# Kernel optimization log

Measured on AMD Instinct MI355X. Metric: run time of the kernel, lower is better.

Reference implementation:

```python
import jax, jax.numpy as jnp
import numpy as np
from jax import lax

# Module config (matches init_kwargs)
KH, KW = 2, 3          # kernel_size
C_IN = 64              # in_channels
C_HID = 256            # hidden_channels (4 * in_channels since in_channels <= 96)
C_OUT = 2 * C_IN       # affine transform -> (mu, log_scale)
DN = ('NCHW', 'OIHW', 'NCHW')


def setup_inputs() -> dict:
    key = jax.random.key(0)
    k0, k1, k2 = jax.random.split(key, 3)
    B, H, W = 32, 64, 64
    x = jax.random.normal(k0, (B, C_IN, H, W), dtype=jnp.float32)
    # masked (shifted) conv weights, order 'A' (height-causal)
    Wm = jax.random.normal(k1, (C_HID, C_IN, KH, KW), dtype=jnp.float32) * 0.05
    bm = jnp.zeros((C_HID,), dtype=jnp.float32)
    # 1x1 projection to transform params
    W1 = jax.random.normal(k2, (C_OUT, C_HID, 1, 1), dtype=jnp.float32) * 0.05
    b1 = jnp.zeros((C_OUT,), dtype=jnp.float32)
    return {"x": x, "Wm": Wm, "bm": bm, "W1": W1, "b1": b1}


def _mcf_block(x, Wm, bm, W1, b1):
    """MCFBlock: shifted masked conv (order 'A') -> ReLU -> 1x1 conv.

    Order 'A' causality: output at (h, w) depends only on input rows
    h-KH .. h-1 (strictly above) and columns w-(KW//2) .. w+(KW//2).
    Implemented by padding KH rows on top, (KW-1)//2 cols on each side,
    dropping the last row, then a VALID conv.
    """
    H = x.shape[2]
    cW = (KW - 1) // 2
    xp = jnp.pad(x, ((0, 0), (0, 0), (KH, 0), (cW, cW)))[:, :, :H + KH - 1]
    c = lax.conv_general_dilated(xp, Wm, (1, 1), 'VALID', dimension_numbers=DN)
    c = jax.nn.relu(c + bm[None, :, None, None])
    p = lax.conv_general_dilated(c, W1, (1, 1), 'VALID', dimension_numbers=DN)
    return p + b1[None, :, None, None]


def reference(x, Wm, bm, W1, b1):
    # params -> (mu, scale) for the affine flow (alpha = 1.0)
    params = _mcf_block(x, Wm, bm, W1, b1)      # [B, 2*C_IN, H, W]
    mu, log_scale = jnp.split(params, 2, axis=1)
    scale = jax.nn.sigmoid(log_scale + 2.0)     # macow affine parameterization
    out = scale * x + mu                        # [B, C_IN, H, W]
    logdet = jnp.sum(jnp.log(scale), axis=(1, 2, 3))  # [B]
    return out, logdet
```

## Files before the change

kernel.cpp:

```cpp
#include <hip/hip_runtime.h>
#include <math.h>


#define BATCH 32
#define HDIM 64
#define WDIM 64
#define ROWS 4
#define STRIPS 16
#define NBLK (BATCH * STRIPS)
#define CT_LD 264

typedef __attribute__((ext_vector_type(8))) short short8;
typedef __attribute__((ext_vector_type(4))) float f32x4;

__device__ inline unsigned short f2bf(float f) {
    union { float f; unsigned int u; } v; v.f = f;
    unsigned int u = v.u;
    unsigned int r = u + 0x7FFFu + ((u >> 16) & 1u);
    return (unsigned short)(r >> 16);
}

__device__ inline int xt_off(int slot, int wp, int ci) {
    return ((slot * 66 + wp) << 6) + ((((ci >> 3) ^ (wp & 7)) << 3) | (ci & 7));
}

__global__ __launch_bounds__(256) void mcf_prep(
    const float* __restrict__ Wm, const float* __restrict__ W1,
    unsigned short* __restrict__ WmR, unsigned short* __restrict__ W1b)
{
    int idx = blockIdx.x * 256 + threadIdx.x;
    if (idx < 6 * 256 * 64) {
        int khkw = idx >> 14;
        int rem = idx & 16383;
        int co = rem >> 6;
        int ci = rem & 63;
        int kh = khkw / 3, kw = khkw % 3;
        WmR[idx] = f2bf(Wm[((co * 64 + ci) * 2 + kh) * 3 + kw]);
    } else {
        int i = idx - 6 * 256 * 64;
        W1b[i] = f2bf(W1[i]);
    }
}

__global__ __launch_bounds__(512, 2) void mcf_mfma(
    const float* __restrict__ x,
    const unsigned short* __restrict__ WmR,
    const float* __restrict__ bm,
    const unsigned short* __restrict__ W1b,
    const float* __restrict__ b1,
    float* __restrict__ out, float* __restrict__ row_ld)
{
    __shared__ __align__(16) unsigned short Xt[5 * 66 * 64];
    __shared__ __align__(16) unsigned short Ct[64 * CT_LD];
    __shared__ float red[8];

    const int blk = blockIdx.x;
    const int b = blk >> 4;
    const int h0 = (blk & 15) * ROWS;
    const int tid = threadIdx.x;
    const int lane = tid & 63;
    const int wv = tid >> 6;
    const int col = lane & 15;
    const int g = lane >> 4;

    for (int l = tid; l < 640; l += 512) {
        int s = l >> 7, rr = l & 127;
        int wp = (rr >= 64) ? 65 : 0, ci = rr & 63;
        Xt[xt_off(s, wp, ci)] = 0;
    }
    #pragma unroll
    for (int it = 0; it < 40; ++it) {
        int idx = it * 512 + tid;
        int w = idx & 63;
        int ci = (idx >> 6) & 63;
        int slot = idx >> 12;
        int row = h0 - 2 + slot;
        float v = 0.f;
        if (row >= 0) v = x[(((size_t)b * 64 + ci) * 64 + row) * 64 + w];
        Xt[xt_off(slot, w + 1, ci)] = f2bf(v);
    }
    __syncthreads();

    float bs1[2][4];
    #pragma unroll
    for (int ct = 0; ct < 2; ++ct)
        #pragma unroll
        for (int j = 0; j < 4; ++j) bs1[ct][j] = bm[wv * 32 + ct * 16 + g * 4 + j];
    const int pr = wv & 3;
    const int wcg = wv >> 2;
    float bMu[4], bLs[4];
    #pragma unroll
    for (int j = 0; j < 4; ++j) {
        bMu[j] = b1[pr * 16 + g * 4 + j];
        bLs[j] = b1[64 + pr * 16 + g * 4 + j];
    }

    float ldacc = 0.f;

    #pragma unroll 1
    for (int r = 0; r < ROWS; ++r) {
        f32x4 acc[2][4];
        #pragma unroll
        for (int ct = 0; ct < 2; ++ct)
            #pragma unroll
            for (int wt = 0; wt < 4; ++wt)
                #pragma unroll
                for (int j = 0; j < 4; ++j) acc[ct][wt][j] = bs1[ct][j];

        #pragma unroll
        for (int kh = 0; kh < 2; ++kh) {
            #pragma unroll
            for (int kw = 0; kw < 3; ++kw) {
                const unsigned short* wmk = WmR + ((kh * 3 + kw) << 14);
                #pragma unroll
                for (int ks = 0; ks < 2; ++ks) {
                    short8 bfrag[4];
                    #pragma unroll
                    for (int wt = 0; wt < 4; ++wt) {
                        int wp = wt * 16 + col + kw;
                        bfrag[wt] = *reinterpret_cast<const short8*>(
                            &Xt[(((r + kh) * 66 + wp) << 6) + ((((ks * 4 + g) ^ (wp & 7)) << 3))]);
                    }
                    #pragma unroll
                    for (int ct = 0; ct < 2; ++ct) {
                        short8 af = *reinterpret_cast<const short8*>(
                            &wmk[(wv * 32 + ct * 16 + col) * 64 + ks * 32 + g * 8]);
                        #pragma unroll
                        for (int wt = 0; wt < 4; ++wt)
                            acc[ct][wt] = __builtin_amdgcn_mfma_f32_16x16x32_bf16(
                                af, bfrag[wt], acc[ct][wt], 0, 0, 0);
                    }
                }
            }
        }
        #pragma unroll
        for (int ct = 0; ct < 2; ++ct) {
            int co_base = wv * 32 + ct * 16 + g * 4;
            #pragma unroll
            for (int wt = 0; wt < 4; ++wt) {
                int w = wt * 16 + col;
                unsigned short pk[4];
                #pragma unroll
                for (int j = 0; j < 4; ++j) pk[j] = f2bf(fmaxf(acc[ct][wt][j], 0.f));
                *reinterpret_cast<unsigned long long*>(&Ct[w * CT_LD + co_base]) =
                    *reinterpret_cast<const unsigned long long*>(pk);
            }
        }
        __syncthreads();

        f32x4 accM[2], accL[2];
        #pragma unroll
        for (int j = 0; j < 4; ++j) {
            accM[0][j] = bMu[j]; accM[1][j] = bMu[j];
            accL[0][j] = bLs[j]; accL[1][j] = bLs[j];
        }
        #pragma unroll
        for (int ks = 0; ks < 8; ++ks) {
            int kk = ks * 32 + g * 8;
            short8 bf2[2];
            #pragma unroll
            for (int wt = 0; wt < 2; ++wt) {
                int w = (wcg * 2 + wt) * 16 + col;
                bf2[wt] = *reinterpret_cast<const short8*>(&Ct[w * CT_LD + kk]);
            }
            int oA = pr * 16 + col;
            short8 aM = *reinterpret_cast<const short8*>(&W1b[oA * 256 + kk]);
            short8 aL = *reinterpret_cast<const short8*>(&W1b[(oA + 64) * 256 + kk]);
            #pragma unroll
            for (int wt = 0; wt < 2; ++wt) {
                accM[wt] = __builtin_amdgcn_mfma_f32_16x16x32_bf16(aM, bf2[wt], accM[wt], 0, 0, 0);
                accL[wt] = __builtin_amdgcn_mfma_f32_16x16x32_bf16(aL, bf2[wt], accL[wt], 0, 0, 0);
            }
        }
        int h = h0 + r;
        #pragma unroll
        for (int wt = 0; wt < 2; ++wt) {
            int w = (wcg * 2 + wt) * 16 + col;
            #pragma unroll
            for (int j = 0; j < 4; ++j) {
                int co = pr * 16 + g * 4 + j;
                float mu = accM[wt][j];
                float ls = accL[wt][j];
                float scale = 1.f / (1.f + __expf(-(ls + 2.f)));
                size_t xi = (((size_t)b * 64 + co) * 64 + h) * 64 + w;
                out[xi] = scale * x[xi] + mu;
                ldacc += __logf(scale);
            }
        }
        __syncthreads();
    }

    #pragma unroll
    for (int off = 32; off; off >>= 1) ldacc += __shfl_down(ldacc, off);
    if (lane == 0) red[wv] = ldacc;
    __syncthreads();
    if (tid == 0) {
        float s = 0.f;
        #pragma unroll
        for (int i = 0; i < 8; ++i) s += red[i];
        row_ld[blk] = s;
    }
}

__global__ __launch_bounds__(64) void mcf_ldreduce(
    const float* __restrict__ row_ld, float* __restrict__ ldout)
{
    int b = blockIdx.x;
    int l = threadIdx.x;
    float v = (l < STRIPS) ? row_ld[b * STRIPS + l] : 0.f;
    #pragma unroll
    for (int off = 32; off; off >>= 1) v += __shfl_down(v, off);
    if (l == 0) ldout[b] = v;
}

extern "C" void kernel_launch(void* const* d_in, const int* in_sizes, int n_in,
                              void* d_out, int out_size, void* d_ws, size_t ws_size,
                              hipStream_t stream) {
    const float* x  = (const float*)d_in[0];
    const float* Wm = (const float*)d_in[1];
    const float* bm = (const float*)d_in[2];
    const float* W1 = (const float*)d_in[3];
    const float* b1 = (const float*)d_in[4];
    float* out = (float*)d_out;

    float* row_ld = (float*)d_ws;
    unsigned short* WmR = (unsigned short*)((char*)d_ws + 8192);
    unsigned short* W1b = WmR + 6 * 256 * 64;

    hipLaunchKernelGGL(mcf_prep, dim3(512), dim3(256), 0, stream,
                       Wm, W1, WmR, W1b);
    hipLaunchKernelGGL(mcf_mfma, dim3(NBLK), dim3(512), 0, stream,
                       x, WmR, bm, W1b, b1, out, row_ld);
    hipLaunchKernelGGL(mcf_ldreduce, dim3(BATCH), dim3(64), 0, stream,
                       row_ld, out + (size_t)BATCH * 64 * HDIM * WDIM);
}
```

Before: 74.72 us.

## Double work-group to 1024 threads, double-buffer Ct, pack Xt loads

Raises the main kernel to 1024 threads (16 waves), so each wave computes 16 hidden channels instead of 32 and one 16-column tile in the projection stage. The Ct buffer is double-buffered by row parity, which removes the second barrier per row. The input staging now loads two channels per thread and writes them as one packed 32-bit LDS store. The aim is more latency hiding and fewer barriers per block, at the cost of more LDS per block and fewer MFMAs per wave to amortize each fragment load.

```diff
diff --git a/kernel.cpp b/kernel.cpp
--- a/kernel.cpp
+++ b/kernel.cpp
@@ -42,7 +42,7 @@
     }
 }
 
-__global__ __launch_bounds__(512, 2) void mcf_mfma(
+__global__ __launch_bounds__(1024, 4) void mcf_mfma(
     const float* __restrict__ x,
     const unsigned short* __restrict__ WmR,
     const float* __restrict__ bm,
@@ -51,8 +51,8 @@
     float* __restrict__ out, float* __restrict__ row_ld)
 {
     __shared__ __align__(16) unsigned short Xt[5 * 66 * 64];
-    __shared__ __align__(16) unsigned short Ct[64 * CT_LD];
-    __shared__ float red[8];
+    __shared__ __align__(16) unsigned short Ct[2][64 * CT_LD];
+    __shared__ float red[16];
 
     const int blk = blockIdx.x;
     const int b = blk >> 4;
@@ -63,31 +63,35 @@
     const int col = lane & 15;
     const int g = lane >> 4;
 
-    for (int l = tid; l < 640; l += 512) {
-        int s = l >> 7, rr = l & 127;
+    if (tid < 640) {
+        int s = tid >> 7, rr = tid & 127;
         int wp = (rr >= 64) ? 65 : 0, ci = rr & 63;
         Xt[xt_off(s, wp, ci)] = 0;
     }
     #pragma unroll
-    for (int it = 0; it < 40; ++it) {
-        int idx = it * 512 + tid;
+    for (int it = 0; it < 10; ++it) {
+        int idx = it * 1024 + tid;
         int w = idx & 63;
-        int ci = (idx >> 6) & 63;
-        int slot = idx >> 12;
+        int ci = ((idx >> 6) & 31) * 2;
+        int slot = idx >> 11;
         int row = h0 - 2 + slot;
-        float v = 0.f;
-        if (row >= 0) v = x[(((size_t)b * 64 + ci) * 64 + row) * 64 + w];
-        Xt[xt_off(slot, w + 1, ci)] = f2bf(v);
+        float v0 = 0.f, v1 = 0.f;
+        if (row >= 0) {
+            const float* base = &x[(((size_t)b * 64 + ci) * 64 + row) * 64 + w];
+            v0 = base[0];
+            v1 = base[64 * 64];
+        }
+        unsigned int pk = (unsigned int)f2bf(v0) | ((unsigned int)f2bf(v1) << 16);
+        *reinterpret_cast<unsigned int*>(&Xt[xt_off(slot, w + 1, ci)]) = pk;
     }
     __syncthreads();
 
-    float bs1[2][4];
-    #pragma unroll
-    for (int ct = 0; ct < 2; ++ct)
-        #pragma unroll
-        for (int j = 0; j < 4; ++j) bs1[ct][j] = bm[wv * 32 + ct * 16 + g * 4 + j];
+    const int co0 = wv * 16;
+    float bs1[4];
+    #pragma unroll
+    for (int j = 0; j < 4; ++j) bs1[j] = bm[co0 + g * 4 + j];
     const int pr = wv & 3;
-    const int wcg = wv >> 2;
+    const int wq = wv >> 2;
     float bMu[4], bLs[4];
     #pragma unroll
     for (int j = 0; j < 4; ++j) {
@@ -99,13 +103,13 @@
 
     #pragma unroll 1
     for (int r = 0; r < ROWS; ++r) {
-        f32x4 acc[2][4];
-        #pragma unroll
-        for (int ct = 0; ct < 2; ++ct)
+        unsigned short* Cb = Ct[r & 1];
+
+        f32x4 acc[4];
+        #pragma unroll
+        for (int wt = 0; wt < 4; ++wt)
             #pragma unroll
-            for (int wt = 0; wt < 4; ++wt)
-                #pragma unroll
-                for (int j = 0; j < 4; ++j) acc[ct][wt][j] = bs1[ct][j];
+            for (int j = 0; j < 4; ++j) acc[wt][j] = bs1[j];
 
         #pragma unroll
         for (int kh = 0; kh < 2; ++kh) {
@@ -114,80 +118,53 @@
                 const unsigned short* wmk = WmR + ((kh * 3 + kw) << 14);
                 #pragma unroll
                 for (int ks = 0; ks < 2; ++ks) {
-                    short8 bfrag[4];
+                    short8 af = *reinterpret_cast<const short8*>(
+                        &wmk[(co0 + col) * 64 + ks * 32 + g * 8]);
                     #pragma unroll
                     for (int wt = 0; wt < 4; ++wt) {
                         int wp = wt * 16 + col + kw;
-                        bfrag[wt] = *reinterpret_cast<const short8*>(
+                        short8 bfrag = *reinterpret_cast<const short8*>(
                             &Xt[(((r + kh) * 66 + wp) << 6) + ((((ks * 4 + g) ^ (wp & 7)) << 3))]);
-                    }
-                    #pragma unroll
-                    for (int ct = 0; ct < 2; ++ct) {
-                        short8 af = *reinterpret_cast<const short8*>(
-                            &wmk[(wv * 32 + ct * 16 + col) * 64 + ks * 32 + g * 8]);
-                        #pragma unroll
-                        for (int wt = 0; wt < 4; ++wt)
-                            acc[ct][wt] = __builtin_amdgcn_mfma_f32_16x16x32_bf16(
-                                af, bfrag[wt], acc[ct][wt], 0, 0, 0);
+                        acc[wt] = __builtin_amdgcn_mfma_f32_16x16x32_bf16(
+                            af, bfrag, acc[wt], 0, 0, 0);
                     }
                 }
             }
         }
         #pragma unroll
-        for (int ct = 0; ct < 2; ++ct) {
-            int co_base = wv * 32 + ct * 16 + g * 4;
+        for (int wt = 0; wt < 4; ++wt) {
+            int w = wt * 16 + col;
+            unsigned short pk[4];
             #pragma unroll
-            for (int wt = 0; wt < 4; ++wt) {
-                int w = wt * 16 + col;
-                unsigned short pk[4];
-                #pragma unroll
-                for (int j = 0; j < 4; ++j) pk[j] = f2bf(fmaxf(acc[ct][wt][j], 0.f));
-                *reinterpret_cast<unsigned long long*>(&Ct[w * CT_LD + co_base]) =
-                    *reinterpret_cast<const unsigned long long*>(pk);
-            }
+            for (int j = 0; j < 4; ++j) pk[j] = f2bf(fmaxf(acc[wt][j], 0.f));
+            *reinterpret_cast<unsigned long long*>(&Cb[w * CT_LD + co0 + g * 4]) =
+                *reinterpret_cast<const unsigned long long*>(pk);
         }
         __syncthreads();
 
-        f32x4 accM[2], accL[2];
-        #pragma unroll
-        for (int j = 0; j < 4; ++j) {
-            accM[0][j] = bMu[j]; accM[1][j] = bMu[j];
-            accL[0][j] = bLs[j]; accL[1][j] = bLs[j];
-        }
+        f32x4 accM, accL;
+        #pragma unroll
+        for (int j = 0; j < 4; ++j) { accM[j] = bMu[j]; accL[j] = bLs[j]; }
+        const int w = wq * 16 + col;
         #pragma unroll
         for (int ks = 0; ks < 8; ++ks) {
             int kk = ks * 32 + g * 8;
-            short8 bf2[2];
-            #pragma unroll
-            for (int wt = 0; wt < 2; ++wt) {
-                int w = (wcg * 2 + wt) * 16 + col;
-                bf2[wt] = *reinterpret_cast<const short8*>(&Ct[w * CT_LD + kk]);
-            }
+            short8 bf2 = *reinterpret_cast<const short8*>(&Cb[w * CT_LD + kk]);
             int oA = pr * 16 + col;
             short8 aM = *reinterpret_cast<const short8*>(&W1b[oA * 256 + kk]);
             short8 aL = *reinterpret_cast<const short8*>(&W1b[(oA + 64) * 256 + kk]);
-            #pragma unroll
-            for (int wt = 0; wt < 2; ++wt) {
-                accM[wt] = __builtin_amdgcn_mfma_f32_16x16x32_bf16(aM, bf2[wt], accM[wt], 0, 0, 0);
-                accL[wt] = __builtin_amdgcn_mfma_f32_16x16x32_bf16(aL, bf2[wt], accL[wt], 0, 0, 0);
-            }
+            accM = __builtin_amdgcn_mfma_f32_16x16x32_bf16(aM, bf2, accM, 0, 0, 0);
+            accL = __builtin_amdgcn_mfma_f32_16x16x32_bf16(aL, bf2, accL, 0, 0, 0);
         }
         int h = h0 + r;
         #pragma unroll
-        for (int wt = 0; wt < 2; ++wt) {
-            int w = (wcg * 2 + wt) * 16 + col;
-            #pragma unroll
-            for (int j = 0; j < 4; ++j) {
-                int co = pr * 16 + g * 4 + j;
-                float mu = accM[wt][j];
-                float ls = accL[wt][j];
-                float scale = 1.f / (1.f + __expf(-(ls + 2.f)));
-                size_t xi = (((size_t)b * 64 + co) * 64 + h) * 64 + w;
-                out[xi] = scale * x[xi] + mu;
-                ldacc += __logf(scale);
-            }
-        }
-        __syncthreads();
+        for (int j = 0; j < 4; ++j) {
+            int co = pr * 16 + g * 4 + j;
+            float scale = 1.f / (1.f + __expf(-(accL[j] + 2.f)));
+            size_t xi = (((size_t)b * 64 + co) * 64 + h) * 64 + w;
+            out[xi] = scale * x[xi] + accM[j];
+            ldacc += __logf(scale);
+        }
     }
 
     #pragma unroll
@@ -197,7 +174,7 @@
     if (tid == 0) {
         float s = 0.f;
         #pragma unroll
-        for (int i = 0; i < 8; ++i) s += red[i];
+        for (int i = 0; i < 16; ++i) s += red[i];
         row_ld[blk] = s;
     }
 }
@@ -229,7 +206,7 @@
 
     hipLaunchKernelGGL(mcf_prep, dim3(512), dim3(256), 0, stream,
                        Wm, W1, WmR, W1b);
-    hipLaunchKernelGGL(mcf_mfma, dim3(NBLK), dim3(512), 0, stream,
+    hipLaunchKernelGGL(mcf_mfma, dim3(NBLK), dim3(1024), 0, stream,
                        x, WmR, bm, W1b, b1, out, row_ld);
     hipLaunchKernelGGL(mcf_ldreduce, dim3(BATCH), dim3(64), 0, stream,
                        row_ld, out + (size_t)BATCH * 64 * HDIM * WDIM);
```

Result: slower. 137.0 us (+83.3%).
